# Kernel tuning notes

Measured on AMD Instinct MI355X. Metric: run time of the kernel, lower is better.

The kernel has to match this reference:

```python
import jax, jax.numpy as jnp
import numpy as np
import math

D_MODEL = 64
D_STATE = 16
IMG = 64
GROUPS = 4
EPS = 1e-5


def group_norm(x, gamma, beta):
    B, C, H, W = x.shape
    xg = x.reshape(B, GROUPS, C // GROUPS, H, W)
    mu = xg.mean(axis=(2, 3, 4), keepdims=True)
    var = ((xg - mu) ** 2).mean(axis=(2, 3, 4), keepdims=True)
    xn = ((xg - mu) * jax.lax.rsqrt(var + EPS)).reshape(B, C, H, W)
    return xn * gamma[None, :, None, None] + beta[None, :, None, None]


def circ_conv(x, w, b=None):
    # 3x3 conv with circular padding, NCHW/OIHW
    xp = jnp.pad(x, ((0, 0), (0, 0), (1, 1), (1, 1)), mode='wrap')
    y = jax.lax.conv_general_dilated(xp, w, window_strides=(1, 1), padding='VALID',
                                     dimension_numbers=('NCHW', 'OIHW', 'NCHW'))
    if b is not None:
        y = y + b[None, :, None, None]
    return y


def setup_inputs() -> dict:
    key = jax.random.key(0)
    ks = jax.random.split(key, 6)
    B = 4
    u_t = jax.random.normal(ks[0], (B, D_MODEL, IMG, IMG), dtype=jnp.float32)
    s_prev = jax.random.normal(ks[1], (B, 3, D_MODEL, D_STATE, IMG, IMG), dtype=jnp.float32)
    gamma = jnp.ones((D_MODEL,), jnp.float32)
    beta = jnp.zeros((D_MODEL,), jnp.float32)
    w_delta = jax.random.normal(ks[2], (D_MODEL, D_MODEL, 3, 3), jnp.float32) * 0.05
    b_delta = jnp.zeros((D_MODEL,), jnp.float32)
    w_B = jax.random.normal(ks[3], (D_STATE, D_MODEL, 3, 3), jnp.float32) * 0.05
    w_C = jax.random.normal(ks[4], (D_STATE, D_MODEL, 3, 3), jnp.float32) * 0.05
    log_A_real = jnp.full((D_MODEL, D_STATE), math.log(0.5), jnp.float32)
    D_param = jnp.ones((D_MODEL,), jnp.float32)
    dt_inv_softplus = jnp.asarray(math.log(math.e - 1.0), jnp.float32)
    return {'u_t': u_t, 's_prev': s_prev, 'gamma': gamma, 'beta': beta,
            'w_delta': w_delta, 'b_delta': b_delta, 'w_B': w_B, 'w_C': w_C,
            'log_A_real': log_A_real, 'D_param': D_param, 'dt_inv_softplus': dt_inv_softplus}


def reference(u_t, s_prev, gamma, beta, w_delta, b_delta, w_B, w_C, log_A_real, D_param, dt_inv_softplus):
    B, D, H, W = u_t.shape
    N = D_STATE
    un = group_norm(u_t, gamma, beta)
    delta = jax.nn.softplus(circ_conv(un, w_delta, b_delta) + dt_inv_softplus)
    delta = jnp.clip(delta, 1e-4, 5.0)                     # [B,D,H,W]
    B_val = circ_conv(un, w_B)                              # [B,N,H,W]
    C_val = circ_conv(un, w_C)                              # [B,N,H,W]
    A = -jnp.exp(log_A_real)                                # [D,N]
    delta_bc = delta[:, :, None]                            # [B,D,1,H,W]
    A_bar = jnp.exp(delta_bc * A[None, :, :, None, None])   # [B,D,N,H,W]
    B_bar = delta_bc * B_val[:, None]                       # [B,D,N,H,W]
    m0, mx, my = s_prev[:, 0], s_prev[:, 1], s_prev[:, 2]   # each [B,D,N,H,W]
    # spectral gradient of m0 over last two (spatial) axes
    ky_ = np.fft.fftfreq(H).astype(np.float32) * 2.0 * np.pi
    kx_ = np.fft.fftfreq(W).astype(np.float32) * 2.0 * np.pi
    ky, kx = jnp.meshgrid(jnp.asarray(ky_), jnp.asarray(kx_), indexing='ij')
    m0f = jnp.fft.fft2(m0)
    grad_y = jnp.fft.ifft2(m0f * (1j * ky)).real
    grad_x = jnp.fft.ifft2(m0f * (1j * kx)).real
    m0_new = A_bar * m0 + B_bar * u_t[:, :, None]
    mx_new = A_bar * (mx - grad_x)
    my_new = A_bar * (my - grad_y)
    s_new = jnp.stack([m0_new, mx_new, my_new], axis=1)     # [B,3,D,N,H,W]
    y_state = jnp.einsum('bdnhw,bnhw->bdhw', m0_new, C_val)
    y_new = (y_state + u_t * D_param[None, :, None, None])[:, None]  # [B,1,D,H,W]
    return (y_new, s_new)
```

## Files before the change

kernel.cpp:

```cpp
#include <hip/hip_runtime.h>
#include <hip/hip_bf16.h>

#define B_ 4
#define D_ 64
#define N_ 16
#define HW_ 4096

#define LDSA 72
#define LDSB 66
#define EXP 68

#define OFF_D2    0u
#define OFF_ATAB  8192u
#define OFF_MEAN  12288u
#define OFF_RSTD  12352u
#define OFF_W9    16384u
#define OFF_UNT   131072u
#define OFF_DELTA 2228224u
#define OFF_BVAL  6422528u
#define OFF_CVAL  7471104u
#define OFF_YBUF  8519680u

typedef __bf16 v8bf __attribute__((ext_vector_type(8)));
typedef float  v4f  __attribute__((ext_vector_type(4)));

__device__ __forceinline__ unsigned short f2bf(float f){
  __hip_bfloat16 h = __float2bfloat16(f);
  return *reinterpret_cast<unsigned short*>(&h);
}
__device__ __forceinline__ v8bf ld8bf(const unsigned short* p){
  union{uint4 u; v8bf v;} c; c.u = *(const uint4*)p; return c.v;
}

__device__ __forceinline__ void bar_lgkm(){
  asm volatile("s_waitcnt lgkmcnt(0)" ::: "memory");
  __builtin_amdgcn_s_barrier();
  __builtin_amdgcn_sched_barrier(0);
}

__global__ void k_init(const float* __restrict__ logA,
                       unsigned short* __restrict__ D2w, float* __restrict__ Atab){
  int g = blockIdx.x*256 + threadIdx.x;
  if(g < 4096){
    int r = g>>6, m = g&63;
    int p = (r - m) & 63;
    float s = 0.f;
    for(int k=1;k<32;k++) s += (float)k * sinf(0.09817477042468103f * (float)(k*p));
    D2w[g] = f2bf(-0.0030679615757712823f * s);
  } else if(g < 5120){
    int idx = g - 4096;
    Atab[idx] = -__expf(logA[idx]);
  }
}

__global__ void k_wrepack(const float* __restrict__ wd,
                          const float* __restrict__ wB,
                          const float* __restrict__ wC,
                          unsigned short* __restrict__ W9){
  int idx = blockIdx.x*256 + threadIdx.x;
  if(idx >= 96*64) return;
  int co = idx>>6, ci = idx&63;
  const float* src;
  if(co < 64)      src = wd + ((size_t)co*64 + ci)*9;
  else if(co < 80) src = wB + ((size_t)(co-64)*64 + ci)*9;
  else             src = wC + ((size_t)(co-80)*64 + ci)*9;
  for(int tap=0; tap<9; tap++)
    W9[((size_t)tap*96 + co)*64 + ci] = f2bf(src[tap]);
}

__global__ void k_gnstats(const float* __restrict__ u,
                          float* __restrict__ meanw, float* __restrict__ rstdw){
  int bg = blockIdx.x;
  const float* base = u + (size_t)bg*65536;
  int t = threadIdx.x;
  float s=0.f, s2=0.f;
  for(int j=0;j<16;j++){
    float4 v = ((const float4*)base)[t + 1024*j];
    s  += v.x+v.y+v.z+v.w;
    s2 += v.x*v.x+v.y*v.y+v.z*v.z+v.w*v.w;
  }
  for(int o=32;o>0;o>>=1){ s += __shfl_down(s,o); s2 += __shfl_down(s2,o); }
  __shared__ float ls[16], ls2[16];
  int wv = t>>6;
  if((t&63)==0){ ls[wv]=s; ls2[wv]=s2; }
  __syncthreads();
  if(t==0){
    float S=0.f,S2=0.f;
    for(int i=0;i<16;i++){ S+=ls[i]; S2+=ls2[i]; }
    float mu = S/65536.f;
    float var = S2/65536.f - mu*mu;
    meanw[bg]=mu; rstdw[bg]=rsqrtf(var+1e-5f);
  }
}

__global__ __launch_bounds__(256) void k_unT(
    const float* __restrict__ u_t,
    const float* __restrict__ meanw, const float* __restrict__ rstdw,
    const float* __restrict__ gamma, const float* __restrict__ beta,
    unsigned short* __restrict__ unT){
  __shared__ unsigned short T[64*LDSA];
  int bid = blockIdx.x;
  int b = bid>>6, h = bid&63;
  int t = threadIdx.x;
  int w = t&63, cg = t>>6;
  #pragma unroll
  for(int i=0;i<16;i++){
    int c = cg*16 + i;
    float x = u_t[(((size_t)b*64 + c)*64 + h)*64 + w];
    int g = c>>4;
    float v = (x - meanw[b*4+g])*rstdw[b*4+g]*gamma[c] + beta[c];
    T[w*LDSA + c] = f2bf(v);
  }
  __syncthreads();
  int w2 = t>>2, cq = t&3;
  uint4 v0 = *(uint4*)&T[w2*LDSA + cq*16];
  uint4 v1 = *(uint4*)&T[w2*LDSA + cq*16 + 8];
  uint4* dst = (uint4*)(unT + ((size_t)b*HW_ + h*64 + w2)*64 + cq*16);
  dst[0] = v0; dst[1] = v1;
}

__global__ __launch_bounds__(256) void k_conv(
    const unsigned short* __restrict__ unT,
    const unsigned short* __restrict__ W9,
    const float* __restrict__ b_d,
    const float* __restrict__ dtp,
    float* __restrict__ deltaw, float* __restrict__ Bvalw, float* __restrict__ Cvalw){
  int bid = blockIdx.x;
  int b = bid>>6, h = bid&63;
  int t = threadIdx.x;
  int wv = t>>6, l = t&63;
  int lr = l&15, lk = l>>4;
  v4f acc[6];
  #pragma unroll
  for(int i=0;i<6;i++) acc[i] = (v4f){0.f,0.f,0.f,0.f};
  int wpix = wv*16 + lr;
  #pragma unroll
  for(int tap=0; tap<9; tap++){
    int dy = tap/3 - 1, dx = tap - (tap/3)*3 - 1;
    int hh = (h+dy)&63;
    int ww = (wpix+dx)&63;
    const unsigned short* bp = unT + ((size_t)b*HW_ + hh*64 + ww)*64;
    const unsigned short* ap = W9 + (size_t)tap*96*64;
    #pragma unroll
    for(int ks=0; ks<2; ks++){
      int k0 = ks*32 + lk*8;
      v8bf bfrag = ld8bf(bp + k0);
      #pragma unroll
      for(int mt=0; mt<6; mt++){
        v8bf afrag = ld8bf(ap + (mt*16+lr)*64 + k0);
        acc[mt] = __builtin_amdgcn_mfma_f32_16x16x32_bf16(afrag, bfrag, acc[mt], 0,0,0);
      }
    }
  }
  float dt = dtp[0];
  int p = h*64 + wpix;
  #pragma unroll
  for(int mt=0; mt<6; mt++){
    #pragma unroll
    for(int r=0;r<4;r++){
      int co = mt*16 + lk*4 + r;
      float v = acc[mt][r];
      if(co < 64){
        float x = v + b_d[co] + dt;
        float sp = (x > 15.f) ? x : log1pf(__expf(x));
        sp = fminf(fmaxf(sp, 1e-4f), 5.f);
        deltaw[((size_t)b*64 + co)*HW_ + p] = sp;
      } else if(co < 80){
        Bvalw[((size_t)b*16 + (co-64))*HW_ + p] = v;
      } else {
        Cvalw[((size_t)b*16 + (co-80))*HW_ + p] = v;
      }
    }
  }
}

__global__ __launch_bounds__(256, 4) void k_main(
    const float* __restrict__ u_t,
    const float* __restrict__ s_prev,
    const unsigned short* __restrict__ D2w,
    const float* __restrict__ Atab,
    const float* __restrict__ deltaw,
    const float* __restrict__ Bvalw,
    const float* __restrict__ Cvalw,
    float* __restrict__ ybuf,
    float* __restrict__ out_s){
  __shared__ __align__(16) unsigned short Mbuf[64*LDSA + 64*LDSB];
  __shared__ __align__(16) unsigned short D2s[64*LDSA];
  unsigned short* Ms72 = Mbuf;
  unsigned short* Ms66 = Mbuf + 64*LDSA;
  float* EX = (float*)Mbuf;

  int bid = blockIdx.x;
  int pair = bid & 255;
  int b = pair & 3, d = pair >> 2;
  int nq = bid >> 8;
  int t = threadIdx.x;
  int wv = t>>6, l = t&63;
  int lr = l & 15, lk = l >> 4;
  int r0 = wv*16;

  size_t bd = (size_t)b*64 + d;
  const size_t PL = (size_t)D_*N_*HW_;
  size_t sbase = (size_t)b*3*PL + (size_t)d*N_*HW_;
  int n0 = nq*4;

  const float* m0base = s_prev + sbase;
  const float* mxbase = s_prev + sbase + PL;
  const float* mybase = s_prev + sbase + 2*PL;

  int g0 = t, g1 = t+256, g2 = t+512, g3 = t+768;

  uint4 d2v0 = ((const uint4*)D2w)[t];
  uint4 d2v1 = ((const uint4*)D2w)[t+256];
  { int r = t>>3, cb = t&7;            *(uint4*)&D2s[r*LDSA + cb*8] = d2v0; }
  { int c2 = t+256; int r = c2>>3, cb = c2&7; *(uint4*)&D2s[r*LDSA + cb*8] = d2v1; }
  const float4* uv4 = (const float4*)(u_t + bd*HW_);
  const float4* dv4 = (const float4*)(deltaw + bd*HW_);
  float4 uq0 = uv4[g0], uq1 = uv4[g1], uq2 = uv4[g2], uq3 = uv4[g3];
  float4 dq0 = dv4[g0], dq1 = dv4[g1], dq2 = dv4[g2], dq3 = dv4[g3];

  float4 yq0 = make_float4(0.f,0.f,0.f,0.f);
  float4 yq1 = yq0, yq2 = yq0, yq3 = yq0;

  for(int ni=0; ni<4; ni++){
    int n = n0 + ni;
    const float4* m0v = (const float4*)(m0base + (size_t)n*HW_);
    float4 pm0 = m0v[g0], pm1 = m0v[g1], pm2 = m0v[g2], pm3 = m0v[g3];
    const float4* mxv = (const float4*)(mxbase + (size_t)n*HW_);
    const float4* myv = (const float4*)(mybase + (size_t)n*HW_);
    float4 sx0 = mxv[g0], sx1 = mxv[g1], sx2 = mxv[g2], sx3 = mxv[g3];
    float4 sy0 = myv[g0], sy1 = myv[g1], sy2 = myv[g2], sy3 = myv[g3];

    #pragma unroll
    for(int j=0;j<4;j++){
      float4 v = (j==0)?pm0:(j==1)?pm1:(j==2)?pm2:pm3;
      int g = t + 256*j;
      int r = g>>4, cb = g&15;
      unsigned int lo = (unsigned int)f2bf(v.x) | ((unsigned int)f2bf(v.y)<<16);
      unsigned int hi = (unsigned int)f2bf(v.z) | ((unsigned int)f2bf(v.w)<<16);
      unsigned int* d72 = (unsigned int*)&Ms72[r*LDSA + cb*4];
      d72[0]=lo; d72[1]=hi;
      unsigned int* d66 = (unsigned int*)&Ms66[r*LDSB + cb*4];
      d66[0]=lo; d66[1]=hi;
    }
    bar_lgkm();

    v4f gxa[4], gya[4];
    #pragma unroll
    for(int ct=0; ct<4; ct++){
      v4f gx = {0.f,0.f,0.f,0.f}, gy = {0.f,0.f,0.f,0.f};
      #pragma unroll
      for(int ks=0; ks<2; ks++){
        int k0 = ks*32 + lk*8;
        v8bf a_gx = ld8bf(&D2s[(ct*16+lr)*LDSA + k0]);
        v8bf b_gx = ld8bf(&Ms72[(r0+lr)*LDSA + k0]);
        gx = __builtin_amdgcn_mfma_f32_16x16x32_bf16(a_gx, b_gx, gx, 0,0,0);
        union { unsigned short s[8]; v8bf v; } ag;
        #pragma unroll
        for(int i=0;i<8;i++) ag.s[i] = Ms66[(k0+i)*LDSB + ct*16 + lr];
        v8bf b_gy = ld8bf(&D2s[(r0+lr)*LDSA + k0]);
        gy = __builtin_amdgcn_mfma_f32_16x16x32_bf16(ag.v, b_gy, gy, 0,0,0);
      }
      gxa[ct] = gx; gya[ct] = gy;
    }
    bar_lgkm();

    #pragma unroll
    for(int ct=0; ct<4; ct++)
      *(v4f*)&EX[(r0+lr)*EXP + (ct*4+lk)*4] = gxa[ct];
    bar_lgkm();
    float4 gxl0 = *(float4*)&EX[(g0>>4)*EXP + (g0&15)*4];
    float4 gxl1 = *(float4*)&EX[(g1>>4)*EXP + (g1&15)*4];
    float4 gxl2 = *(float4*)&EX[(g2>>4)*EXP + (g2&15)*4];
    float4 gxl3 = *(float4*)&EX[(g3>>4)*EXP + (g3&15)*4];
    bar_lgkm();
    #pragma unroll
    for(int ct=0; ct<4; ct++)
      *(v4f*)&EX[(r0+lr)*EXP + (ct*4+lk)*4] = gya[ct];
    bar_lgkm();

    float An = Atab[d*16 + n];
    const float4* Bv  = (const float4*)(Bvalw + ((size_t)b*16 + n)*HW_);
    const float4* Cv  = (const float4*)(Cvalw + ((size_t)b*16 + n)*HW_);
    float* so = out_s + sbase + (size_t)n*HW_;
    float4* so0 = (float4*)so;
    float4* so1 = (float4*)(so + PL);
    float4* so2 = (float4*)(so + 2*PL);

    #pragma unroll
    for(int k=0; k<4; k++){
      int g = t + 256*k;
      float4 B4  = Bv[g];
      float4 C4  = Cv[g];
      float4 gyl = *(float4*)&EX[(g>>4)*EXP + (g&15)*4];
      float4 gxl = (k==0)?gxl0:(k==1)?gxl1:(k==2)?gxl2:gxl3;
      float4 m04 = (k==0)?pm0:(k==1)?pm1:(k==2)?pm2:pm3;
      float4 mx4 = (k==0)?sx0:(k==1)?sx1:(k==2)?sx2:sx3;
      float4 my4 = (k==0)?sy0:(k==1)?sy1:(k==2)?sy2:sy3;
      float4 u4  = (k==0)?uq0:(k==1)?uq1:(k==2)?uq2:uq3;
      float4 dv_ = (k==0)?dq0:(k==1)?dq1:(k==2)?dq2:dq3;
      float4 ab, m0n, mxn, myn;
      ab.x = __expf(dv_.x*An);
      ab.y = __expf(dv_.y*An);
      ab.z = __expf(dv_.z*An);
      ab.w = __expf(dv_.w*An);
      m0n.x = ab.x*m04.x + dv_.x*B4.x*u4.x;
      m0n.y = ab.y*m04.y + dv_.y*B4.y*u4.y;
      m0n.z = ab.z*m04.z + dv_.z*B4.z*u4.z;
      m0n.w = ab.w*m04.w + dv_.w*B4.w*u4.w;
      mxn.x = ab.x*(mx4.x - gxl.x);
      mxn.y = ab.y*(mx4.y - gxl.y);
      mxn.z = ab.z*(mx4.z - gxl.z);
      mxn.w = ab.w*(mx4.w - gxl.w);
      myn.x = ab.x*(my4.x - gyl.x);
      myn.y = ab.y*(my4.y - gyl.y);
      myn.z = ab.z*(my4.z - gyl.z);
      myn.w = ab.w*(my4.w - gyl.w);
      if(k==0){ yq0.x += m0n.x*C4.x; yq0.y += m0n.y*C4.y; yq0.z += m0n.z*C4.z; yq0.w += m0n.w*C4.w; }
      if(k==1){ yq1.x += m0n.x*C4.x; yq1.y += m0n.y*C4.y; yq1.z += m0n.z*C4.z; yq1.w += m0n.w*C4.w; }
      if(k==2){ yq2.x += m0n.x*C4.x; yq2.y += m0n.y*C4.y; yq2.z += m0n.z*C4.z; yq2.w += m0n.w*C4.w; }
      if(k==3){ yq3.x += m0n.x*C4.x; yq3.y += m0n.y*C4.y; yq3.z += m0n.z*C4.z; yq3.w += m0n.w*C4.w; }
      so0[g] = m0n;
      so1[g] = mxn;
      so2[g] = myn;
    }
    __syncthreads();
  }

  float* yb = ybuf + bd*HW_;
  #pragma unroll
  for(int k=0; k<4; k++){
    int p = 4*(t + 256*k);
    float4 yv = (k==0)?yq0:(k==1)?yq1:(k==2)?yq2:yq3;
    atomicAdd(&yb[p+0], yv.x);
    atomicAdd(&yb[p+1], yv.y);
    atomicAdd(&yb[p+2], yv.z);
    atomicAdd(&yb[p+3], yv.w);
  }
}

__global__ void k_y(const float* __restrict__ ybuf,
                    const float* __restrict__ u_t,
                    const float* __restrict__ Dp,
                    float* __restrict__ out_y){
  int i = blockIdx.x*blockDim.x + threadIdx.x;
  int d = (i>>10)&63;
  float Dv = Dp[d];
  float4 uv = ((const float4*)u_t)[i];
  float4 yv = ((const float4*)ybuf)[i];
  float4 o;
  o.x = yv.x + uv.x*Dv;
  o.y = yv.y + uv.y*Dv;
  o.z = yv.z + uv.z*Dv;
  o.w = yv.w + uv.w*Dv;
  ((float4*)out_y)[i] = o;
}

extern "C" void kernel_launch(void* const* d_in, const int* in_sizes, int n_in,
                              void* d_out, int out_size, void* d_ws, size_t ws_size,
                              hipStream_t stream){
  const float* u_t    = (const float*)d_in[0];
  const float* s_prev = (const float*)d_in[1];
  const float* gamma  = (const float*)d_in[2];
  const float* beta   = (const float*)d_in[3];
  const float* w_d    = (const float*)d_in[4];
  const float* b_d    = (const float*)d_in[5];
  const float* w_B    = (const float*)d_in[6];
  const float* w_C    = (const float*)d_in[7];
  const float* logA   = (const float*)d_in[8];
  const float* Dp     = (const float*)d_in[9];
  const float* dtp    = (const float*)d_in[10];

  char* ws = (char*)d_ws;
  unsigned short* D2w  = (unsigned short*)(ws + OFF_D2);
  float* Atab          = (float*)(ws + OFF_ATAB);
  float* meanw         = (float*)(ws + OFF_MEAN);
  float* rstdw         = (float*)(ws + OFF_RSTD);
  unsigned short* W9   = (unsigned short*)(ws + OFF_W9);
  unsigned short* unT  = (unsigned short*)(ws + OFF_UNT);
  float* deltaw        = (float*)(ws + OFF_DELTA);
  float* Bvalw         = (float*)(ws + OFF_BVAL);
  float* Cvalw         = (float*)(ws + OFF_CVAL);
  float* ybuf          = (float*)(ws + OFF_YBUF);

  float* out_y = (float*)d_out;
  float* out_s = out_y + 1048576;

  hipMemsetAsync(ws + OFF_YBUF, 0, 4u*1048576u, stream);
  k_init   <<<20, 256, 0, stream>>>(logA, D2w, Atab);
  k_wrepack<<<24, 256, 0, stream>>>(w_d, w_B, w_C, W9);
  k_gnstats<<<16, 1024, 0, stream>>>(u_t, meanw, rstdw);
  k_unT    <<<256, 256, 0, stream>>>(u_t, meanw, rstdw, gamma, beta, unT);
  k_conv   <<<256, 256, 0, stream>>>(unT, W9, b_d, dtp, deltaw, Bvalw, Cvalw);
  k_main   <<<1024, 256, 0, stream>>>(u_t, s_prev, D2w, Atab, deltaw, Bvalw, Cvalw, ybuf, out_s);
  k_y      <<<1024, 256, 0, stream>>>(ybuf, u_t, Dp, out_y);
}
```

Baseline: 188.0 us.

## Keep gradient operator in registers, double-buffer LDS, store gradients as bf16

The D2 spectral-derivative operator fragments now live in registers instead of an LDS tile. The LDS state buffer is double-buffered so the gradient exchange can reuse the other half, which removes several barriers per iteration. Gradients are packed to bf16 in LDS so gx and gy are exchanged together, and u/delta are reloaded per iteration rather than held in registers. The trade is more VGPRs, which may reduce occupancy, plus an extra bf16 rounding of the gradients.

New measurement: 200.5 us. 6.6% more time.

```diff
diff --git a/kernel.cpp b/kernel.cpp
--- a/kernel.cpp
+++ b/kernel.cpp
@@ -8,7 +8,8 @@
 
 #define LDSA 72
 #define LDSB 66
-#define EXP 68
+#define MSZ  (64*LDSA + 64*LDSB)
+#define EXPU 68
 
 #define OFF_D2    0u
 #define OFF_ATAB  8192u
@@ -27,6 +28,9 @@
 __device__ __forceinline__ unsigned short f2bf(float f){
   __hip_bfloat16 h = __float2bfloat16(f);
   return *reinterpret_cast<unsigned short*>(&h);
+}
+__device__ __forceinline__ float bf2f(unsigned int u){
+  union{unsigned int i; float f;} c; c.i = (u & 0xffffu)<<16; return c.f;
 }
 __device__ __forceinline__ v8bf ld8bf(const unsigned short* p){
   union{uint4 u; v8bf v;} c; c.u = *(const uint4*)p; return c.v;
@@ -184,11 +188,7 @@
     const float* __restrict__ Cvalw,
     float* __restrict__ ybuf,
     float* __restrict__ out_s){
-  __shared__ __align__(16) unsigned short Mbuf[64*LDSA + 64*LDSB];
-  __shared__ __align__(16) unsigned short D2s[64*LDSA];
-  unsigned short* Ms72 = Mbuf;
-  unsigned short* Ms66 = Mbuf + 64*LDSA;
-  float* EX = (float*)Mbuf;
+  __shared__ __align__(16) unsigned short Mbuf[2][MSZ];
 
   int bid = blockIdx.x;
   int pair = bid & 255;
@@ -210,20 +210,31 @@
 
   int g0 = t, g1 = t+256, g2 = t+512, g3 = t+768;
 
-  uint4 d2v0 = ((const uint4*)D2w)[t];
-  uint4 d2v1 = ((const uint4*)D2w)[t+256];
-  { int r = t>>3, cb = t&7;            *(uint4*)&D2s[r*LDSA + cb*8] = d2v0; }
-  { int c2 = t+256; int r = c2>>3, cb = c2&7; *(uint4*)&D2s[r*LDSA + cb*8] = d2v1; }
+  v8bf d2gx[8];
+  v8bf d2gy[2];
+  #pragma unroll
+  for(int ct=0; ct<4; ct++)
+    #pragma unroll
+    for(int ks=0; ks<2; ks++)
+      d2gx[ct*2+ks] = ld8bf(D2w + (ct*16+lr)*64 + ks*32 + lk*8);
+  #pragma unroll
+  for(int ks=0; ks<2; ks++)
+    d2gy[ks] = ld8bf(D2w + (r0+lr)*64 + ks*32 + lk*8);
+
   const float4* uv4 = (const float4*)(u_t + bd*HW_);
   const float4* dv4 = (const float4*)(deltaw + bd*HW_);
-  float4 uq0 = uv4[g0], uq1 = uv4[g1], uq2 = uv4[g2], uq3 = uv4[g3];
-  float4 dq0 = dv4[g0], dq1 = dv4[g1], dq2 = dv4[g2], dq3 = dv4[g3];
 
   float4 yq0 = make_float4(0.f,0.f,0.f,0.f);
   float4 yq1 = yq0, yq2 = yq0, yq3 = yq0;
 
   for(int ni=0; ni<4; ni++){
     int n = n0 + ni;
+    int cur = ni & 1;
+    unsigned short* Ms72c = Mbuf[cur];
+    unsigned short* Ms66c = Mbuf[cur] + 64*LDSA;
+    unsigned short* EXx   = Mbuf[cur^1];
+    unsigned short* EXy   = Mbuf[cur^1] + 64*EXPU;
+
     const float4* m0v = (const float4*)(m0base + (size_t)n*HW_);
     float4 pm0 = m0v[g0], pm1 = m0v[g1], pm2 = m0v[g2], pm3 = m0v[g3];
     const float4* mxv = (const float4*)(mxbase + (size_t)n*HW_);
@@ -238,45 +249,34 @@
       int r = g>>4, cb = g&15;
       unsigned int lo = (unsigned int)f2bf(v.x) | ((unsigned int)f2bf(v.y)<<16);
       unsigned int hi = (unsigned int)f2bf(v.z) | ((unsigned int)f2bf(v.w)<<16);
-      unsigned int* d72 = (unsigned int*)&Ms72[r*LDSA + cb*4];
+      unsigned int* d72 = (unsigned int*)&Ms72c[r*LDSA + cb*4];
       d72[0]=lo; d72[1]=hi;
-      unsigned int* d66 = (unsigned int*)&Ms66[r*LDSB + cb*4];
+      unsigned int* d66 = (unsigned int*)&Ms66c[r*LDSB + cb*4];
       d66[0]=lo; d66[1]=hi;
     }
     bar_lgkm();
 
-    v4f gxa[4], gya[4];
     #pragma unroll
     for(int ct=0; ct<4; ct++){
       v4f gx = {0.f,0.f,0.f,0.f}, gy = {0.f,0.f,0.f,0.f};
       #pragma unroll
       for(int ks=0; ks<2; ks++){
         int k0 = ks*32 + lk*8;
-        v8bf a_gx = ld8bf(&D2s[(ct*16+lr)*LDSA + k0]);
-        v8bf b_gx = ld8bf(&Ms72[(r0+lr)*LDSA + k0]);
-        gx = __builtin_amdgcn_mfma_f32_16x16x32_bf16(a_gx, b_gx, gx, 0,0,0);
+        v8bf b_gx = ld8bf(&Ms72c[(r0+lr)*LDSA + k0]);
+        gx = __builtin_amdgcn_mfma_f32_16x16x32_bf16(d2gx[ct*2+ks], b_gx, gx, 0,0,0);
         union { unsigned short s[8]; v8bf v; } ag;
         #pragma unroll
-        for(int i=0;i<8;i++) ag.s[i] = Ms66[(k0+i)*LDSB + ct*16 + lr];
-        v8bf b_gy = ld8bf(&D2s[(r0+lr)*LDSA + k0]);
-        gy = __builtin_amdgcn_mfma_f32_16x16x32_bf16(ag.v, b_gy, gy, 0,0,0);
+        for(int i=0;i<8;i++) ag.s[i] = Ms66c[(k0+i)*LDSB + ct*16 + lr];
+        gy = __builtin_amdgcn_mfma_f32_16x16x32_bf16(ag.v, d2gy[ks], gy, 0,0,0);
       }
-      gxa[ct] = gx; gya[ct] = gy;
-    }
-    bar_lgkm();
-
-    #pragma unroll
-    for(int ct=0; ct<4; ct++)
-      *(v4f*)&EX[(r0+lr)*EXP + (ct*4+lk)*4] = gxa[ct];
-    bar_lgkm();
-    float4 gxl0 = *(float4*)&EX[(g0>>4)*EXP + (g0&15)*4];
-    float4 gxl1 = *(float4*)&EX[(g1>>4)*EXP + (g1&15)*4];
-    float4 gxl2 = *(float4*)&EX[(g2>>4)*EXP + (g2&15)*4];
-    float4 gxl3 = *(float4*)&EX[(g3>>4)*EXP + (g3&15)*4];
-    bar_lgkm();
-    #pragma unroll
-    for(int ct=0; ct<4; ct++)
-      *(v4f*)&EX[(r0+lr)*EXP + (ct*4+lk)*4] = gya[ct];
+      int eo = (r0+lr)*EXPU + (ct*4+lk)*4;
+      unsigned int x0 = (unsigned int)f2bf(gx[0]) | ((unsigned int)f2bf(gx[1])<<16);
+      unsigned int x1 = (unsigned int)f2bf(gx[2]) | ((unsigned int)f2bf(gx[3])<<16);
+      *(uint2*)&EXx[eo] = make_uint2(x0,x1);
+      unsigned int y0 = (unsigned int)f2bf(gy[0]) | ((unsigned int)f2bf(gy[1])<<16);
+      unsigned int y1 = (unsigned int)f2bf(gy[2]) | ((unsigned int)f2bf(gy[3])<<16);
+      *(uint2*)&EXy[eo] = make_uint2(y0,y1);
+    }
     bar_lgkm();
 
     float An = Atab[d*16 + n];
@@ -292,13 +292,14 @@
       int g = t + 256*k;
       float4 B4  = Bv[g];
       float4 C4  = Cv[g];
-      float4 gyl = *(float4*)&EX[(g>>4)*EXP + (g&15)*4];
-      float4 gxl = (k==0)?gxl0:(k==1)?gxl1:(k==2)?gxl2:gxl3;
+      float4 u4  = uv4[g];
+      float4 dv_ = dv4[g];
+      int eo = (g>>4)*EXPU + (g&15)*4;
+      uint2 ux = *(const uint2*)&EXx[eo];
+      uint2 uy = *(const uint2*)&EXy[eo];
       float4 m04 = (k==0)?pm0:(k==1)?pm1:(k==2)?pm2:pm3;
       float4 mx4 = (k==0)?sx0:(k==1)?sx1:(k==2)?sx2:sx3;
       float4 my4 = (k==0)?sy0:(k==1)?sy1:(k==2)?sy2:sy3;
-      float4 u4  = (k==0)?uq0:(k==1)?uq1:(k==2)?uq2:uq3;
-      float4 dv_ = (k==0)?dq0:(k==1)?dq1:(k==2)?dq2:dq3;
       float4 ab, m0n, mxn, myn;
       ab.x = __expf(dv_.x*An);
       ab.y = __expf(dv_.y*An);
@@ -308,14 +309,14 @@
       m0n.y = ab.y*m04.y + dv_.y*B4.y*u4.y;
       m0n.z = ab.z*m04.z + dv_.z*B4.z*u4.z;
       m0n.w = ab.w*m04.w + dv_.w*B4.w*u4.w;
-      mxn.x = ab.x*(mx4.x - gxl.x);
-      mxn.y = ab.y*(mx4.y - gxl.y);
-      mxn.z = ab.z*(mx4.z - gxl.z);
-      mxn.w = ab.w*(mx4.w - gxl.w);
-      myn.x = ab.x*(my4.x - gyl.x);
-      myn.y = ab.y*(my4.y - gyl.y);
-      myn.z = ab.z*(my4.z - gyl.z);
-      myn.w = ab.w*(my4.w - gyl.w);
+      mxn.x = ab.x*(mx4.x - bf2f(ux.x));
+      mxn.y = ab.y*(mx4.y - bf2f(ux.x>>16));
+      mxn.z = ab.z*(mx4.z - bf2f(ux.y));
+      mxn.w = ab.w*(mx4.w - bf2f(ux.y>>16));
+      myn.x = ab.x*(my4.x - bf2f(uy.x));
+      myn.y = ab.y*(my4.y - bf2f(uy.x>>16));
+      myn.z = ab.z*(my4.z - bf2f(uy.y));
+      myn.w = ab.w*(my4.w - bf2f(uy.y>>16));
       if(k==0){ yq0.x += m0n.x*C4.x; yq0.y += m0n.y*C4.y; yq0.z += m0n.z*C4.z; yq0.w += m0n.w*C4.w; }
       if(k==1){ yq1.x += m0n.x*C4.x; yq1.y += m0n.y*C4.y; yq1.z += m0n.z*C4.z; yq1.w += m0n.w*C4.w; }
       if(k==2){ yq2.x += m0n.x*C4.x; yq2.y += m0n.y*C4.y; yq2.z += m0n.z*C4.z; yq2.w += m0n.w*C4.w; }
```
